# Kernel tuning notes

Measured on AMD Instinct MI355X. Metric: run time of the kernel, lower is better.

## Reference

```python
import jax, jax.numpy as jnp
import numpy as np

K = 32
BN_EPS = 1e-5


def _edgeconv(x, W, b):
    # x: [N, f] one point cloud; dynamic kNN in feature space (self included,
    # matching torch_geometric knn), edge feature [x_i, x_j - x_i], linear MLP,
    # max aggregation over the k neighbors.
    sq = jnp.sum(x * x, axis=1)                      # [N]
    dist = sq[:, None] + sq[None, :] - 2.0 * (x @ x.T)  # [N, N] squared dists
    _, idx = jax.lax.top_k(-dist, K)                 # [N, K] nearest (incl. self)
    xj = x[idx]                                      # [N, K, f]
    xi = jnp.broadcast_to(x[:, None, :], xj.shape)   # [N, K, f]
    e = jnp.concatenate([xi, xj - xi], axis=-1)      # [N, K, 2f]
    m = jnp.einsum('nkf,fo->nko', e, W) + b          # [N, K, o]
    return jnp.max(m, axis=1)                        # [N, o]


def _relu_bn(y, gamma, beta):
    # Sequential(ReLU(), BatchNorm1d(o)) in training mode over flattened nodes.
    a = jax.nn.relu(y)                               # [B, N, o]
    B, N, o = a.shape
    flat = a.reshape(B * N, o)
    mean = jnp.mean(flat, axis=0)
    var = jnp.var(flat, axis=0)
    norm = (flat - mean) * jax.lax.rsqrt(var + BN_EPS)
    return (norm * gamma + beta).reshape(B, N, o)


def setup_inputs() -> dict:
    key = jax.random.key(0)
    ks = jax.random.split(key, 4)
    B, N, fin = 8, 4096, 3
    x = jax.random.normal(ks[0], (B, N, fin), dtype=jnp.float32)
    target = jax.random.normal(ks[1], (B, N, fin), dtype=jnp.float32)
    # MLP(2*i, o) weights for layer dims (3->64), (64->64), (64->3)
    W1 = jax.random.normal(ks[2], (6, 64), dtype=jnp.float32) * (1.0 / np.sqrt(6))
    b1 = jnp.zeros((64,), jnp.float32)
    g1 = jnp.ones((64,), jnp.float32)
    be1 = jnp.zeros((64,), jnp.float32)
    W2 = jax.random.normal(ks[3], (128, 64), dtype=jnp.float32) * (1.0 / np.sqrt(128))
    b2 = jnp.zeros((64,), jnp.float32)
    g2 = jnp.ones((64,), jnp.float32)
    be2 = jnp.zeros((64,), jnp.float32)
    W3 = jax.random.normal(jax.random.fold_in(key, 7), (128, 3), dtype=jnp.float32) * (1.0 / np.sqrt(128))
    b3 = jnp.zeros((3,), jnp.float32)
    return {"x": x, "target": target, "W1": W1, "b1": b1, "g1": g1, "be1": be1,
            "W2": W2, "b2": b2, "g2": g2, "be2": be2, "W3": W3, "b3": b3}


def reference(x, target, W1, b1, g1, be1, W2, b2, g2, be2, W3, b3):
    ec = jax.vmap(_edgeconv, in_axes=(0, None, None))
    h = ec(x, W1, b1)                 # [B, N, 64]
    h = _relu_bn(h, g1, be1)
    h = ec(h, W2, b2)                 # [B, N, 64]
    h = _relu_bn(h, g2, be2)
    h = ec(h, W3, b3)                 # [B, N, 3], last activation = Identity
    loss = jnp.mean((h - target) ** 2)
    return (h, loss)
```

## Files before the change

### kernel.cpp

```cpp
#include <hip/hip_runtime.h>
#include <cstdint>
#include <cstddef>

static constexpr int NPTS  = 4096;
static constexpr int NB    = 8;
static constexpr int NROWS = NB * NPTS;
static constexpr int KNN   = 32;
static constexpr int CAP   = 384;
static constexpr int QCAP  = 96;

typedef __attribute__((ext_vector_type(8))) short  bf16x8;
typedef __attribute__((ext_vector_type(4))) float  f32x4;

__device__ __forceinline__ unsigned long long shfl_xor_u64(unsigned long long v, int m) {
  int lo = __shfl_xor((int)(unsigned)(v & 0xFFFFFFFFULL), m, 64);
  int hi = __shfl_xor((int)(unsigned)(v >> 32), m, 64);
  return ((unsigned long long)(unsigned)hi << 32) | (unsigned)lo;
}
__device__ __forceinline__ unsigned long long shfl_u64(unsigned long long v, int src) {
  int lo = __shfl((int)(unsigned)(v & 0xFFFFFFFFULL), src, 64);
  int hi = __shfl((int)(unsigned)(v >> 32), src, 64);
  return ((unsigned long long)(unsigned)hi << 32) | (unsigned)lo;
}

__device__ __forceinline__ unsigned f2o(float f) {
  unsigned u = __float_as_uint(f);
  return (u & 0x80000000u) ? ~u : (u | 0x80000000u);
}
__device__ __forceinline__ float o2f(unsigned o) {
  unsigned u = (o & 0x80000000u) ? (o ^ 0x80000000u) : ~o;
  return __uint_as_float(u);
}

__global__ __launch_bounds__(256) void sqnorm_kernel(const float* __restrict__ x,
                                                     float* __restrict__ sq, int F) {
  int t = blockIdx.x * 256 + threadIdx.x;
  if (t >= NROWS) return;
  const float* p = x + (size_t)t * F;
  float s = 0.f;
  for (int f = 0; f < F; ++f) s = fmaf(p[f], p[f], s);
  sq[t] = s;
}

__global__ __launch_bounds__(256) void split_kernel(const float* __restrict__ x,
                                                    unsigned short* __restrict__ hi,
                                                    unsigned short* __restrict__ lo,
                                                    int total) {
  int t = blockIdx.x * 256 + threadIdx.x;
  if (t >= total) return;
  float v = x[t];
  unsigned u = __float_as_uint(v);
  unsigned h = (u + 0x7FFFu + ((u >> 16) & 1u)) >> 16;
  float hf = __uint_as_float(h << 16);
  float r = v - hf;
  unsigned ur = __float_as_uint(r);
  unsigned l = (ur + 0x7FFFu + ((ur >> 16) & 1u)) >> 16;

  const int n = t >> 6;
  const int f = t & 63;
  const int b   = n >> 12;
  const int g   = (n >> 4) & 255;
  const int l16 = n & 15;
  const int p    = f >> 5;
  const int quad = (f >> 3) & 3;
  const int w    = f & 7;
  const size_t dst = ((((size_t)b * 256 + g) * 2 + p) << 9)
                   + (size_t)(quad * 16 + l16) * 8 + w;
  hi[dst] = (unsigned short)h;
  lo[dst] = (unsigned short)l;
}

__global__ __launch_bounds__(256) void batchmax_kernel(const float* __restrict__ sq,
                                                       float* __restrict__ sqmax) {
  int b = blockIdx.x, t = threadIdx.x;
  float m = 0.f;
  for (int i = t; i < NPTS; i += 256) m = fmaxf(m, sq[b * NPTS + i]);
  for (int off = 32; off >= 1; off >>= 1) m = fmaxf(m, __shfl_xor(m, off, 64));
  __shared__ float ls[4];
  if ((t & 63) == 0) ls[t >> 6] = m;
  __syncthreads();
  if (t == 0) sqmax[b] = fmaxf(fmaxf(ls[0], ls[1]), fmaxf(ls[2], ls[3]));
}

__global__ __launch_bounds__(256, 4)
void knn_screen(const unsigned short* __restrict__ hi,
                const unsigned short* __restrict__ lo,
                const float* __restrict__ sq,
                const float* __restrict__ sqmax,
                int* __restrict__ gcnt,
                unsigned short* __restrict__ glist) {
  const int t = threadIdx.x, wave = t >> 6, lane = t & 63;
  const int l16 = lane & 15, quad = lane >> 4;
  const int bid = blockIdx.x;
  const int b    = bid & 7;
  const int qtr  = (bid >> 3) & 3;
  const int i0w  = ((bid >> 5) << 6) + (wave << 4);
  const int cbq  = qtr << 10;
  const size_t base = (size_t)b * NPTS;
  const unsigned short* hib = hi + base * 64;
  const unsigned short* lob = lo + base * 64;
  const float* sqb = sq + base;
  const float sqm = sqmax[b];
  const int laneoff = lane * 8;

  bf16x8 ahi[2], alo[2];
#pragma unroll
  for (int kb = 0; kb < 2; ++kb) {
    const size_t abase = ((size_t)((i0w >> 4) * 2 + kb) << 9);
    ahi[kb] = *(const bf16x8*)(hib + abase + laneoff);
    alo[kb] = *(const bf16x8*)(lob + abase + laneoff);
  }
  float sqi4[4];
#pragma unroll
  for (int reg = 0; reg < 4; ++reg) sqi4[reg] = sqb[i0w + quad * 4 + reg];

  float t1[4], t2[4], t3[4], t4[4], tinf4[4];
  int cnt4[4] = {0, 0, 0, 0};
#pragma unroll
  for (int reg = 0; reg < 4; ++reg) {
    t1[reg] = 3.4e38f; t2[reg] = 3.4e38f; t3[reg] = 3.4e38f; t4[reg] = 3.4e38f;
    tinf4[reg] = 0.f;
  }

#pragma unroll 2
  for (int sub = 0; sub < 64; ++sub) {
    const size_t bb = ((size_t)((qtr * 64 + sub) * 2) << 9);
    bf16x8 bh0 = *(const bf16x8*)(hib + bb + laneoff);
    bf16x8 bh1 = *(const bf16x8*)(hib + bb + 512 + laneoff);
    bf16x8 bl0 = *(const bf16x8*)(lob + bb + laneoff);
    bf16x8 bl1 = *(const bf16x8*)(lob + bb + 512 + laneoff);
    f32x4 acc = {0.f, 0.f, 0.f, 0.f};
    acc = __builtin_amdgcn_mfma_f32_16x16x32_bf16(ahi[0], bh0, acc, 0, 0, 0);
    acc = __builtin_amdgcn_mfma_f32_16x16x32_bf16(ahi[1], bh1, acc, 0, 0, 0);
    acc = __builtin_amdgcn_mfma_f32_16x16x32_bf16(ahi[0], bl0, acc, 0, 0, 0);
    acc = __builtin_amdgcn_mfma_f32_16x16x32_bf16(ahi[1], bl1, acc, 0, 0, 0);
    acc = __builtin_amdgcn_mfma_f32_16x16x32_bf16(alo[0], bh0, acc, 0, 0, 0);
    acc = __builtin_amdgcn_mfma_f32_16x16x32_bf16(alo[1], bh1, acc, 0, 0, 0);
    const float cs = sqb[cbq + sub * 16 + l16];
#pragma unroll
    for (int reg = 0; reg < 4; ++reg) {
      float d = fmaf(-2.f, acc[reg], sqi4[reg] + cs);
      float m1 = fminf(d,  t1[reg]); float M1 = fmaxf(d,  t1[reg]);
      float m2 = fminf(M1, t2[reg]); float M2 = fmaxf(M1, t2[reg]);
      float m3 = fminf(M2, t3[reg]); float M3 = fmaxf(M2, t3[reg]);
      t1[reg] = m1; t2[reg] = m2; t3[reg] = m3;
      t4[reg] = fminf(M3, t4[reg]);
    }
  }

#pragma unroll
  for (int reg = 0; reg < 4; ++reg) {
    unsigned c0s = f2o(t1[reg]);
    unsigned c1s = f2o(t2[reg]);
    unsigned c2s = f2o(t3[reg]);
    unsigned c3s = f2o(t4[reg]);
    unsigned prefix = 0;
    int need = 32;
    for (int bit = 31; bit >= 0; --bit) {
      unsigned hm = (bit == 31) ? 0u : ~((1u << (bit + 1)) - 1u);
      bool a0 = (((c0s ^ prefix) & hm) == 0u) && (((c0s >> bit) & 1u) == 0u);
      bool a1 = (((c1s ^ prefix) & hm) == 0u) && (((c1s >> bit) & 1u) == 0u);
      bool a2 = (((c2s ^ prefix) & hm) == 0u) && (((c2s >> bit) & 1u) == 0u);
      bool a3 = (((c3s ^ prefix) & hm) == 0u) && (((c3s >> bit) & 1u) == 0u);
      unsigned long long b0 = __ballot(a0);
      unsigned long long b1 = __ballot(a1);
      unsigned long long b2 = __ballot(a2);
      unsigned long long b3 = __ballot(a3);
      int cnt0 = __popc((unsigned)((b0 >> (quad * 16)) & 0xFFFFULL))
               + __popc((unsigned)((b1 >> (quad * 16)) & 0xFFFFULL))
               + __popc((unsigned)((b2 >> (quad * 16)) & 0xFFFFULL))
               + __popc((unsigned)((b3 >> (quad * 16)) & 0xFFFFULL));
      if (cnt0 < need) { need -= cnt0; prefix |= 1u << bit; }
    }
    float T = o2f(prefix);
    float eps = 6e-5f * (sqi4[reg] + sqm) + 1e-5f;
    tinf4[reg] = T + 2.f * eps;
  }

#pragma unroll 2
  for (int sub = 0; sub < 64; ++sub) {
    const size_t bb = ((size_t)((qtr * 64 + sub) * 2) << 9);
    bf16x8 bh0 = *(const bf16x8*)(hib + bb + laneoff);
    bf16x8 bh1 = *(const bf16x8*)(hib + bb + 512 + laneoff);
    bf16x8 bl0 = *(const bf16x8*)(lob + bb + laneoff);
    bf16x8 bl1 = *(const bf16x8*)(lob + bb + 512 + laneoff);
    f32x4 acc = {0.f, 0.f, 0.f, 0.f};
    acc = __builtin_amdgcn_mfma_f32_16x16x32_bf16(ahi[0], bh0, acc, 0, 0, 0);
    acc = __builtin_amdgcn_mfma_f32_16x16x32_bf16(ahi[1], bh1, acc, 0, 0, 0);
    acc = __builtin_amdgcn_mfma_f32_16x16x32_bf16(ahi[0], bl0, acc, 0, 0, 0);
    acc = __builtin_amdgcn_mfma_f32_16x16x32_bf16(ahi[1], bl1, acc, 0, 0, 0);
    acc = __builtin_amdgcn_mfma_f32_16x16x32_bf16(alo[0], bh0, acc, 0, 0, 0);
    acc = __builtin_amdgcn_mfma_f32_16x16x32_bf16(alo[1], bh1, acc, 0, 0, 0);
    const int jg0 = cbq + sub * 16 + l16;
    const float cs = sqb[jg0];
#pragma unroll
    for (int reg = 0; reg < 4; ++reg) {
      float d = fmaf(-2.f, acc[reg], sqi4[reg] + cs);
      bool keep = d <= tinf4[reg];
      unsigned long long mask = __ballot(keep);
      unsigned qm = (unsigned)((mask >> (quad * 16)) & 0xFFFFULL);
      if (qm) {
        int rank = __popc(qm & ((1u << l16) - 1u));
        if (keep) {
          int pos = cnt4[reg] + rank;
          if (pos < QCAP)
            glist[(size_t)(base + i0w + quad * 4 + reg) * CAP + qtr * QCAP + pos] =
                (unsigned short)jg0;
        }
        cnt4[reg] += __popc(qm);
      }
    }
  }

  if (l16 == 0) {
#pragma unroll
    for (int reg = 0; reg < 4; ++reg)
      gcnt[(base + i0w + quad * 4 + reg) * 4 + qtr] = cnt4[reg];
  }
}

__global__ __launch_bounds__(256, 2)
void knn_rerank(const float* __restrict__ x, const float* __restrict__ sq,
                const int* __restrict__ gcnt,
                const unsigned short* __restrict__ glist,
                unsigned short* __restrict__ idx_out) {
  const int t = threadIdx.x, wave = t >> 6, lane = t & 63;
  const int row = blockIdx.x * 4 + wave;
  const int b = row >> 12;
  const int i = row & (NPTS - 1);
  const float* xb  = x + (size_t)b * NPTS * 64;
  const float* sqb = sq + ((size_t)b << 12);

  const int n0 = gcnt[row * 4 + 0];
  const int n1 = gcnt[row * 4 + 1];
  const int n2 = gcnt[row * 4 + 2];
  const int n3 = gcnt[row * 4 + 3];
  if (n0 > QCAP || n1 > QCAP || n2 > QCAP || n3 > QCAP) return;

  const float sqi = sqb[i];
  float4 q[16];
#pragma unroll
  for (int c4 = 0; c4 < 16; ++c4)
    q[c4] = *(const float4*)(xb + (size_t)i * 64 + c4 * 4);

  const int n01  = n0 + n1;
  const int n012 = n01 + n2;
  const int n    = n012 + n3;
  unsigned long long vk[6];
#pragma unroll
  for (int s = 0; s < 6; ++s) {
    int li = s * 64 + lane;
    unsigned long long v = 0xFFFFFFFFFFFULL;
    if (li < n) {
      int sl = (li < n0)   ? li
             : (li < n01)  ? QCAP     + (li - n0)
             : (li < n012) ? 2 * QCAP + (li - n01)
                           : 3 * QCAP + (li - n012);
      int j = glist[(size_t)row * CAP + sl];
      const float4* xj = (const float4*)(xb + (size_t)j * 64);
      float dot = 0.f;
#pragma unroll
      for (int c4 = 0; c4 < 16; ++c4) {
        float4 c = xj[c4];
        dot = fmaf(q[c4].x, c.x, dot);
        dot = fmaf(q[c4].y, c.y, dot);
        dot = fmaf(q[c4].z, c.z, dot);
        dot = fmaf(q[c4].w, c.w, dot);
      }
      float d = fmaf(-2.f, dot, sqi + sqb[j]);
      unsigned u  = __float_as_uint(d);
      unsigned ck = (u & 0x80000000u) ? ~u : (u | 0x80000000u);
      v = ((unsigned long long)ck << 12) | (unsigned)j;
    }
    vk[s] = v;
  }
  unsigned long long prefix = 0;
  int need = 32;
  for (int bit = 43; bit >= 0; --bit) {
    unsigned long long hm = (bit == 43) ? 0ULL
        : (~((1ULL << (bit + 1)) - 1ULL) & 0xFFFFFFFFFFFULL);
    int cnt0 = 0;
#pragma unroll
    for (int s = 0; s < 6; ++s) {
      bool a = ((vk[s] ^ prefix) & hm) == 0ULL;
      bool z = ((vk[s] >> bit) & 1ULL) == 0ULL;
      cnt0 += (int)__popcll(__ballot(a && z));
    }
    if (cnt0 < need) { need -= cnt0; prefix |= 1ULL << bit; }
  }
  int prev = 0;
#pragma unroll
  for (int s = 0; s < 6; ++s) {
    bool sel = vk[s] <= prefix;
    unsigned long long m = __ballot(sel);
    int rank = (int)__popcll(m & ((1ULL << lane) - 1ULL));
    if (sel)
      idx_out[(size_t)row * KNN + prev + rank] =
          (unsigned short)(vk[s] & 0xFFFULL);
    prev += (int)__popcll(m);
  }
}

__global__ __launch_bounds__(256)
void knn_rerank_fb(const float* __restrict__ x, const float* __restrict__ sq,
                   const int* __restrict__ gcnt,
                   unsigned short* __restrict__ idx_out) {
  __shared__ unsigned long long fsurv[4][128];
  const int t = threadIdx.x, wave = t >> 6, lane = t & 63;
  const int row = blockIdx.x * 4 + wave;
  const int b = row >> 12;
  const int i = row & (NPTS - 1);

  const int n0 = gcnt[row * 4 + 0];
  const int n1 = gcnt[row * 4 + 1];
  const int n2 = gcnt[row * 4 + 2];
  const int n3 = gcnt[row * 4 + 3];
  if (n0 <= QCAP && n1 <= QCAP && n2 <= QCAP && n3 <= QCAP) return;

  const float* xb  = x + (size_t)b * NPTS * 64;
  const float* sqb = sq + ((size_t)b << 12);
  const float sqi = sqb[i];

  float4 q[16];
#pragma unroll
  for (int c4 = 0; c4 < 16; ++c4)
    q[c4] = *(const float4*)(xb + (size_t)i * 64 + c4 * 4);

  unsigned mnf = 0xFFFFFFFFu;
  for (int c0 = 0; c0 < NPTS; c0 += 64) {
    const int j = c0 + lane;
    const float4* xj = (const float4*)(xb + (size_t)j * 64);
    float dot = 0.f;
#pragma unroll
    for (int c4 = 0; c4 < 16; ++c4) {
      float4 c = xj[c4];
      dot = fmaf(q[c4].x, c.x, dot);
      dot = fmaf(q[c4].y, c.y, dot);
      dot = fmaf(q[c4].z, c.z, dot);
      dot = fmaf(q[c4].w, c.w, dot);
    }
    float d = fmaf(-2.f, dot, sqi + sqb[j]);
    unsigned u  = __float_as_uint(d);
    unsigned ck = (u & 0x80000000u) ? ~u : (u | 0x80000000u);
    mnf = ck < mnf ? ck : mnf;
  }
  unsigned tau32;
  {
    const unsigned v = mnf;
    unsigned prefix32 = 0;
    int need = 32;
    int act = 1;
    for (int bit = 31; bit >= 0; --bit) {
      const unsigned bv = (v >> bit) & 1u;
      unsigned long long m0 = __ballot(act && (bv == 0u));
      int c0n = (int)__popcll(m0);
      if (c0n >= need) {
        act = act && (bv == 0u);
      } else {
        need -= c0n;
        act = act && (bv == 1u);
        prefix32 |= (1u << bit);
      }
    }
    tau32 = prefix32;
  }
  int cnt = 0;
  for (int c0 = 0; c0 < NPTS; c0 += 64) {
    const int j = c0 + lane;
    const float4* xj = (const float4*)(xb + (size_t)j * 64);
    float dot = 0.f;
#pragma unroll
    for (int c4 = 0; c4 < 16; ++c4) {
      float4 c = xj[c4];
      dot = fmaf(q[c4].x, c.x, dot);
      dot = fmaf(q[c4].y, c.y, dot);
      dot = fmaf(q[c4].z, c.z, dot);
      dot = fmaf(q[c4].w, c.w, dot);
    }
    float d = fmaf(-2.f, dot, sqi + sqb[j]);
    unsigned u  = __float_as_uint(d);
    unsigned ck = (u & 0x80000000u) ? ~u : (u | 0x80000000u);
    bool keep = ck <= tau32;
    unsigned long long mask = __ballot(keep);
    if (mask != 0ULL) {
      int rank = (int)__popcll(mask & ((1ULL << lane) - 1ULL));
      if (keep) {
        int pos = cnt + rank;
        if (pos < 128)
          fsurv[wave][pos] = ((unsigned long long)ck << 12) | (unsigned)j;
      }
      cnt += (int)__popcll(mask);
    }
  }
  if (cnt <= 128) {
    unsigned long long vk0 = (lane      < cnt) ? fsurv[wave][lane]      : 0xFFFFFFFFFFFULL;
    unsigned long long vk1 = (lane + 64 < cnt) ? fsurv[wave][lane + 64] : 0xFFFFFFFFFFFULL;
    unsigned long long prefix = 0;
    int need = 32;
    for (int bit = 43; bit >= 0; --bit) {
      unsigned long long hm = (bit == 43) ? 0ULL
          : (~((1ULL << (bit + 1)) - 1ULL) & 0xFFFFFFFFFFFULL);
      bool a0 = (((vk0 ^ prefix) & hm) == 0ULL) && (((vk0 >> bit) & 1ULL) == 0ULL);
      bool a1 = (((vk1 ^ prefix) & hm) == 0ULL) && (((vk1 >> bit) & 1ULL) == 0ULL);
      int cnt0 = (int)__popcll(__ballot(a0)) + (int)__popcll(__ballot(a1));
      if (cnt0 < need) { need -= cnt0; prefix |= 1ULL << bit; }
    }
    bool sel0 = vk0 <= prefix;
    unsigned long long m0 = __ballot(sel0);
    int rank0 = (int)__popcll(m0 & ((1ULL << lane) - 1ULL));
    if (sel0)
      idx_out[(size_t)row * KNN + rank0] = (unsigned short)(vk0 & 0xFFFULL);
    int prev = (int)__popcll(m0);
    bool sel1 = vk1 <= prefix;
    unsigned long long m1 = __ballot(sel1);
    int rank1 = (int)__popcll(m1 & ((1ULL << lane) - 1ULL));
    if (sel1)
      idx_out[(size_t)row * KNN + prev + rank1] = (unsigned short)(vk1 & 0xFFFULL);
  } else {
    unsigned long long ent = (0xFFFFFFFFFFFULL << 5) | (unsigned long long)(lane & 31);
    unsigned long long M   = (0xFFFFFFFFFFFULL << 5) | 31ULL;
    for (int c0 = 0; c0 < NPTS; c0 += 64) {
      const int j = c0 + lane;
      const float4* xj = (const float4*)(xb + (size_t)j * 64);
      float dot = 0.f;
#pragma unroll
      for (int c4 = 0; c4 < 16; ++c4) {
        float4 c = xj[c4];
        dot = fmaf(q[c4].x, c.x, dot);
        dot = fmaf(q[c4].y, c.y, dot);
        dot = fmaf(q[c4].z, c.z, dot);
        dot = fmaf(q[c4].w, c.w, dot);
      }
      float d = fmaf(-2.f, dot, sqi + sqb[j]);
      unsigned u  = __float_as_uint(d);
      unsigned ck = (u & 0x80000000u) ? ~u : (u | 0x80000000u);
      unsigned long long cq = ((unsigned long long)ck << 12) | (unsigned)j;
      unsigned long long mask = __ballot(cq < (M >> 5));
      while (mask) {
        const int src = __builtin_ctzll(mask);
        mask &= mask - 1;
        const unsigned long long bq = shfl_u64(cq, src);
        if (bq < (M >> 5)) {
          const unsigned slot = (unsigned)(M & 31ULL);
          if ((unsigned)(lane & 31) == slot) ent = (bq << 5) | slot;
          unsigned long long v = ent;
#pragma unroll
          for (int off = 16; off >= 1; off >>= 1) {
            unsigned long long w2 = shfl_xor_u64(v, off);
            v = (v > w2) ? v : w2;
          }
          M = v;
        }
      }
    }
    if (lane < 32)
      idx_out[(size_t)row * KNN + lane] =
          (unsigned short)((ent >> 5) & 0xFFFULL);
  }
}

template <int F>
__global__ __launch_bounds__(256, 4) void knn_tiled(const float* __restrict__ x,
                                                    const float* __restrict__ sq,
                                                    unsigned short* __restrict__ idx_out) {
  constexpr int FP = 4;
  constexpr int TC = 256;
  constexpr int RPB = 32;
  constexpr int RPW = 8;
  constexpr int SCAP = 128;

  __shared__ __attribute__((aligned(16))) float qv[RPB][FP];
  __shared__ float qsq[RPB];
  __shared__ __attribute__((aligned(16))) float ct[TC][FP];
  __shared__ float csq[TC];
  __shared__ unsigned long long surv[RPB][SCAP];

  const int t    = threadIdx.x;
  const int wave = t >> 6;
  const int lane = t & 63;
  const int rowbase = blockIdx.x << 5;
  const int b     = rowbase >> 12;
  const int ibase = rowbase & (NPTS - 1);
  const float* xb  = x + (size_t)b * NPTS * F;
  const float* sqb = sq + (b << 12);

  if (t < RPB) {
    qv[t][0] = xb[(size_t)(ibase + t) * 3 + 0];
    qv[t][1] = xb[(size_t)(ibase + t) * 3 + 1];
    qv[t][2] = xb[(size_t)(ibase + t) * 3 + 2];
    qv[t][3] = 0.f;
    qsq[t] = sqb[ibase + t];
  }
  __syncthreads();

  const int r0 = wave << 3;
  float4 q[RPW];
  float sqi[RPW];
#pragma unroll
  for (int rr = 0; rr < RPW; ++rr) {
    q[rr] = *reinterpret_cast<const float4*>(&qv[r0 + rr][0]);
    sqi[rr] = qsq[r0 + rr];
  }

  unsigned mn[RPW];
#pragma unroll
  for (int rr = 0; rr < RPW; ++rr) mn[rr] = 0xFFFFFFFFu;

  for (int tile = 0; tile < NPTS / TC; ++tile) {
    __syncthreads();
    {
      int jg = tile * TC + t;
      ct[t][0] = xb[(size_t)jg * 3 + 0];
      ct[t][1] = xb[(size_t)jg * 3 + 1];
      ct[t][2] = xb[(size_t)jg * 3 + 2];
      ct[t][3] = 0.f;
      csq[t] = sqb[jg];
    }
    __syncthreads();

    float4 c0 = *reinterpret_cast<const float4*>(&ct[lane][0]);
    float4 c1 = *reinterpret_cast<const float4*>(&ct[lane + 64][0]);
    float4 c2 = *reinterpret_cast<const float4*>(&ct[lane + 128][0]);
    float4 c3 = *reinterpret_cast<const float4*>(&ct[lane + 192][0]);
    float cs[4];
#pragma unroll
    for (int s = 0; s < 4; ++s) cs[s] = csq[lane + 64 * s];

#pragma unroll
    for (int rr = 0; rr < RPW; ++rr) {
      float4 qq = q[rr];
      float dd[4];
      dd[0] = fmaf(qq.z, c0.z, fmaf(qq.y, c0.y, qq.x * c0.x));
      dd[1] = fmaf(qq.z, c1.z, fmaf(qq.y, c1.y, qq.x * c1.x));
      dd[2] = fmaf(qq.z, c2.z, fmaf(qq.y, c2.y, qq.x * c2.x));
      dd[3] = fmaf(qq.z, c3.z, fmaf(qq.y, c3.y, qq.x * c3.x));
#pragma unroll
      for (int s = 0; s < 4; ++s) {
        float d = fmaf(-2.f, dd[s], sqi[rr] + cs[s]);
        unsigned u  = __float_as_uint(d);
        unsigned ck = (u & 0x80000000u) ? ~u : (u | 0x80000000u);
        mn[rr] = ck < mn[rr] ? ck : mn[rr];
      }
    }
  }

  unsigned tau[RPW];
#pragma unroll
  for (int rr = 0; rr < RPW; ++rr) {
    const unsigned v = mn[rr];
    unsigned prefix = 0;
    int need = 32;
    int act = 1;
    for (int bit = 31; bit >= 0; --bit) {
      const unsigned bv = (v >> bit) & 1u;
      unsigned long long m0 = __ballot(act && (bv == 0u));
      int c0n = (int)__popcll(m0);
      if (c0n >= need) {
        act = act && (bv == 0u);
      } else {
        need -= c0n;
        act = act && (bv == 1u);
        prefix |= (1u << bit);
      }
    }
    tau[rr] = prefix;
  }

  int cnt[RPW];
#pragma unroll
  for (int rr = 0; rr < RPW; ++rr) cnt[rr] = 0;

  for (int tile = 0; tile < NPTS / TC; ++tile) {
    __syncthreads();
    {
      int jg = tile * TC + t;
      ct[t][0] = xb[(size_t)jg * 3 + 0];
      ct[t][1] = xb[(size_t)jg * 3 + 1];
      ct[t][2] = xb[(size_t)jg * 3 + 2];
      ct[t][3] = 0.f;
      csq[t] = sqb[jg];
    }
    __syncthreads();

    float4 c0 = *reinterpret_cast<const float4*>(&ct[lane][0]);
    float4 c1 = *reinterpret_cast<const float4*>(&ct[lane + 64][0]);
    float4 c2 = *reinterpret_cast<const float4*>(&ct[lane + 128][0]);
    float4 c3 = *reinterpret_cast<const float4*>(&ct[lane + 192][0]);
    float cs[4];
#pragma unroll
    for (int s = 0; s < 4; ++s) cs[s] = csq[lane + 64 * s];

#pragma unroll
    for (int rr = 0; rr < RPW; ++rr) {
      float4 qq = q[rr];
      float dd[4];
      dd[0] = fmaf(qq.z, c0.z, fmaf(qq.y, c0.y, qq.x * c0.x));
      dd[1] = fmaf(qq.z, c1.z, fmaf(qq.y, c1.y, qq.x * c1.x));
      dd[2] = fmaf(qq.z, c2.z, fmaf(qq.y, c2.y, qq.x * c2.x));
      dd[3] = fmaf(qq.z, c3.z, fmaf(qq.y, c3.y, qq.x * c3.x));
#pragma unroll
      for (int s = 0; s < 4; ++s) {
        float d = fmaf(-2.f, dd[s], sqi[rr] + cs[s]);
        unsigned u  = __float_as_uint(d);
        unsigned ck = (u & 0x80000000u) ? ~u : (u | 0x80000000u);
        bool keep = ck <= tau[rr];
        unsigned long long mask = __ballot(keep);
        if (mask != 0ULL) {
          int rank = (int)__popcll(mask & ((1ULL << lane) - 1ULL));
          if (keep) {
            int pos = cnt[rr] + rank;
            if (pos < SCAP)
              surv[r0 + rr][pos] =
                  ((unsigned long long)ck << 12) |
                  (unsigned)(tile * TC + s * 64 + lane);
          }
          cnt[rr] += (int)__popcll(mask);
        }
      }
    }
  }

#pragma unroll
  for (int rr = 0; rr < RPW; ++rr) {
    const int row = rowbase + r0 + rr;
    const int n = cnt[rr];
    if (n <= SCAP) {
      unsigned long long vk0 = (lane      < n) ? surv[r0 + rr][lane]      : 0xFFFFFFFFFFFULL;
      unsigned long long vk1 = (lane + 64 < n) ? surv[r0 + rr][lane + 64] : 0xFFFFFFFFFFFULL;
      unsigned long long prefix = 0;
      int need = 32;
      for (int bit = 43; bit >= 0; --bit) {
        unsigned long long hm = (bit == 43) ? 0ULL
            : (~((1ULL << (bit + 1)) - 1ULL) & 0xFFFFFFFFFFFULL);
        bool a0 = (((vk0 ^ prefix) & hm) == 0ULL) && (((vk0 >> bit) & 1ULL) == 0ULL);
        bool a1 = (((vk1 ^ prefix) & hm) == 0ULL) && (((vk1 >> bit) & 1ULL) == 0ULL);
        int cnt0 = (int)__popcll(__ballot(a0)) + (int)__popcll(__ballot(a1));
        if (cnt0 < need) { need -= cnt0; prefix |= 1ULL << bit; }
      }
      bool sel0 = vk0 <= prefix;
      unsigned long long m0 = __ballot(sel0);
      int rank0 = (int)__popcll(m0 & ((1ULL << lane) - 1ULL));
      if (sel0)
        idx_out[(row << 5) + rank0] = (unsigned short)(vk0 & 0xFFFULL);
      int prev = (int)__popcll(m0);
      bool sel1 = vk1 <= prefix;
      unsigned long long m1 = __ballot(sel1);
      int rank1 = (int)__popcll(m1 & ((1ULL << lane) - 1ULL));
      if (sel1)
        idx_out[(row << 5) + prev + rank1] = (unsigned short)(vk1 & 0xFFFULL);
    } else {
      unsigned long long ent = (0xFFFFFFFFFFFULL << 5) | (unsigned long long)(lane & 31);
      unsigned long long M   = (0xFFFFFFFFFFFULL << 5) | 31ULL;
      const float4 qq = q[rr];
      const float si = sqi[rr];
      for (int c0i = 0; c0i < NPTS; c0i += 64) {
        const int j = c0i + lane;
        const float dd_ = fmaf(qq.z, xb[(size_t)j * 3 + 2],
                           fmaf(qq.y, xb[(size_t)j * 3 + 1],
                                qq.x * xb[(size_t)j * 3 + 0]));
        float d = fmaf(-2.f, dd_, si + sqb[j]);
        unsigned u  = __float_as_uint(d);
        unsigned ck = (u & 0x80000000u) ? ~u : (u | 0x80000000u);
        unsigned long long cq = ((unsigned long long)ck << 12) | (unsigned)j;
        unsigned long long mask = __ballot(cq < (M >> 5));
        while (mask) {
          const int src = __builtin_ctzll(mask);
          mask &= mask - 1;
          const unsigned long long bq = shfl_u64(cq, src);
          if (bq < (M >> 5)) {
            const unsigned slot = (unsigned)(M & 31ULL);
            if ((unsigned)(lane & 31) == slot) ent = (bq << 5) | slot;
            unsigned long long v = ent;
#pragma unroll
            for (int off = 16; off >= 1; off >>= 1) {
              unsigned long long w2 = shfl_xor_u64(v, off);
              v = (v > w2) ? v : w2;
            }
            M = v;
          }
        }
      }
      if (lane < 32)
        idx_out[(row << 5) + lane] = (unsigned short)((ent >> 5) & 0xFFFULL);
    }
  }
}

__global__ __launch_bounds__(256) void mlp_pc_kernel(const float* __restrict__ xin,
                                                     const float* __restrict__ W,
                                                     const float* __restrict__ bias,
                                                     float* __restrict__ P,
                                                     float* C,
                                                     int F, int O, int total) {
  int t = blockIdx.x * 256 + threadIdx.x;
  if (t >= total) return;
  int n = t / O, o = t % O;
  const float* xr = xin + (size_t)n * F;
  const float* Wt = W + o;
  const float* Wb = W + (size_t)F * O + o;
  float p = 0.f, c = 0.f;
  for (int f = 0; f < F; ++f) {
    float a  = xr[f];
    float wt = Wt[(size_t)f * O];
    float wb = Wb[(size_t)f * O];
    p = fmaf(a, wb, p);
    c = fmaf(a, wt - wb, c);
  }
  P[t] = p;
  C[t] = c + bias[o];
}

__global__ __launch_bounds__(256) void aggregate_kernel(const unsigned short* __restrict__ idx,
                                                        const float* __restrict__ P,
                                                        float* h, int O, int total) {
  int t = blockIdx.x * 256 + threadIdx.x;
  if (t >= total) return;
  int n = t / O, o = t % O;
  const unsigned short* ix = idx + (size_t)n * KNN;
  const int rowbase = (n >> 12) << 12;
  float m = -3.402823466e+38f;
  for (int k = 0; k < KNN; ++k) {
    int jg = rowbase + ix[k];
    float v = P[(size_t)jg * O + o];
    m = fmaxf(m, v);
  }
  h[t] = h[t] + m;
}

__global__ __launch_bounds__(256) void bn_stats_kernel(const float* __restrict__ h,
                                                       float* __restrict__ stats) {
  const int c = blockIdx.x;
  const int t = threadIdx.x;
  double s = 0.0, s2 = 0.0;
  for (int n = t; n < NROWS; n += 256) {
    float v = h[(size_t)n * 64 + c];
    v = v > 0.f ? v : 0.f;
    s += v;
    s2 += (double)v * v;
  }
  __shared__ double ls[256], ls2[256];
  ls[t] = s; ls2[t] = s2;
  __syncthreads();
  for (int st = 128; st; st >>= 1) {
    if (t < st) { ls[t] += ls[t + st]; ls2[t] += ls2[t + st]; }
    __syncthreads();
  }
  if (t == 0) {
    double mean = ls[0] / (double)NROWS;
    double var  = ls2[0] / (double)NROWS - mean * mean;
    stats[c]      = (float)mean;
    stats[64 + c] = (float)(1.0 / sqrt(var + 1e-5));
  }
}

__global__ __launch_bounds__(256) void bn_apply_kernel(const float* h,
                                                       const float* __restrict__ stats,
                                                       const float* __restrict__ g,
                                                       const float* __restrict__ be,
                                                       float* out, int total) {
  int t = blockIdx.x * 256 + threadIdx.x;
  if (t >= total) return;
  int ch = t & 63;
  float v = fmaxf(h[t], 0.f);
  out[t] = (v - stats[ch]) * stats[64 + ch] * g[ch] + be[ch];
}

__global__ __launch_bounds__(256) void final_kernel(const float* __restrict__ h3,
                                                    const float* __restrict__ target,
                                                    float* __restrict__ out,
                                                    double* __restrict__ partial) {
  double s = 0.0;
  for (int t = blockIdx.x * 256 + threadIdx.x; t < NROWS * 3; t += 256 * 256) {
    float v = h3[t];
    out[t] = v;
    float d = v - target[t];
    s += (double)d * d;
  }
  __shared__ double ls[256];
  int t = threadIdx.x;
  ls[t] = s;
  __syncthreads();
  for (int st = 128; st; st >>= 1) {
    if (t < st) ls[t] += ls[t + st];
    __syncthreads();
  }
  if (t == 0) partial[blockIdx.x] = ls[0];
}

__global__ __launch_bounds__(256) void loss_kernel(const double* __restrict__ partial,
                                                   float* __restrict__ out) {
  int t = threadIdx.x;
  __shared__ double ls[256];
  ls[t] = partial[t];
  __syncthreads();
  for (int st = 128; st; st >>= 1) {
    if (t < st) ls[t] += ls[t + st];
    __syncthreads();
  }
  if (t == 0) out[NROWS * 3] = (float)(ls[0] / (double)(NROWS * 3));
}

extern "C" void kernel_launch(void* const* d_in, const int* in_sizes, int n_in,
                              void* d_out, int out_size, void* d_ws, size_t ws_size,
                              hipStream_t stream) {
  const float* x   = (const float*)d_in[0];
  const float* tgt = (const float*)d_in[1];
  const float* W1  = (const float*)d_in[2];
  const float* b1  = (const float*)d_in[3];
  const float* g1  = (const float*)d_in[4];
  const float* be1 = (const float*)d_in[5];
  const float* W2  = (const float*)d_in[6];
  const float* b2  = (const float*)d_in[7];
  const float* g2  = (const float*)d_in[8];
  const float* be2 = (const float*)d_in[9];
  const float* W3  = (const float*)d_in[10];
  const float* b3  = (const float*)d_in[11];
  float* out = (float*)d_out;

  char* ws = (char*)d_ws;
  size_t off = 0;
  float* sq    = (float*)(ws + off); off += (size_t)NROWS * 4;
  unsigned short* idxb = (unsigned short*)(ws + off); off += (size_t)NROWS * KNN * 2;
  float* P     = (float*)(ws + off); off += (size_t)NROWS * 64 * 4;
  float* CA    = (float*)(ws + off); off += (size_t)NROWS * 64 * 4;
  float* CB    = (float*)(ws + off); off += (size_t)NROWS * 64 * 4;
  int*   gcnt  = (int*)(ws + off);   off += (size_t)NROWS * 16;
  unsigned short* glist = (unsigned short*)(ws + off); off += (size_t)NROWS * CAP * 2;
  float* stats = (float*)(ws + off); off += 256 * 4;
  float* sqmax = (float*)(ws + off); off += 64;
  double* part = (double*)(ws + off); off += 256 * 8;

  unsigned short* hib = (unsigned short*)P;
  unsigned short* lob = hib + (size_t)NROWS * 64;

  const int T64 = NROWS * 64;
  const int T3  = NROWS * 3;

  sqnorm_kernel<<<NROWS / 256, 256, 0, stream>>>(x, sq, 3);
  knn_tiled<3><<<NROWS / 32, 256, 0, stream>>>(x, sq, idxb);
  mlp_pc_kernel<<<T64 / 256, 256, 0, stream>>>(x, W1, b1, P, CA, 3, 64, T64);
  aggregate_kernel<<<T64 / 256, 256, 0, stream>>>(idxb, P, CA, 64, T64);
  bn_stats_kernel<<<64, 256, 0, stream>>>(CA, stats);
  bn_apply_kernel<<<T64 / 256, 256, 0, stream>>>(CA, stats, g1, be1, CA, T64);

  sqnorm_kernel<<<NROWS / 256, 256, 0, stream>>>(CA, sq, 64);
  split_kernel<<<T64 / 256, 256, 0, stream>>>(CA, hib, lob, T64);
  batchmax_kernel<<<NB, 256, 0, stream>>>(sq, sqmax);
  knn_screen<<<2048, 256, 0, stream>>>(hib, lob, sq, sqmax, gcnt, glist);
  knn_rerank<<<NROWS / 4, 256, 0, stream>>>(CA, sq, gcnt, glist, idxb);
  knn_rerank_fb<<<NROWS / 4, 256, 0, stream>>>(CA, sq, gcnt, idxb);
  mlp_pc_kernel<<<T64 / 256, 256, 0, stream>>>(CA, W2, b2, P, CB, 64, 64, T64);
  aggregate_kernel<<<T64 / 256, 256, 0, stream>>>(idxb, P, CB, 64, T64);
  bn_stats_kernel<<<64, 256, 0, stream>>>(CB, stats);
  bn_apply_kernel<<<T64 / 256, 256, 0, stream>>>(CB, stats, g2, be2, CB, T64);

  sqnorm_kernel<<<NROWS / 256, 256, 0, stream>>>(CB, sq, 64);
  split_kernel<<<T64 / 256, 256, 0, stream>>>(CB, hib, lob, T64);
  batchmax_kernel<<<NB, 256, 0, stream>>>(sq, sqmax);
  knn_screen<<<2048, 256, 0, stream>>>(hib, lob, sq, sqmax, gcnt, glist);
  knn_rerank<<<NROWS / 4, 256, 0, stream>>>(CB, sq, gcnt, glist, idxb);
  knn_rerank_fb<<<NROWS / 4, 256, 0, stream>>>(CB, sq, gcnt, idxb);
  mlp_pc_kernel<<<T3 / 256, 256, 0, stream>>>(CB, W3, b3, P, CA, 64, 3, T3);
  aggregate_kernel<<<T3 / 256, 256, 0, stream>>>(idxb, P, CA, 3, T3);

  final_kernel<<<256, 256, 0, stream>>>(CA, tgt, out, part);
  loss_kernel<<<1, 256, 0, stream>>>(part, out);
}
```

Baseline: 1.478 ms.

## Split kNN candidate screening into halves instead of quarters

The screening kernel now splits the candidate columns into two halves of 2048 points instead of four quarters of 1024. Each query row then keeps a top-4-per-lane threshold over more candidates. That gives a tighter cut, so fewer candidates survive into a smaller 256-slot list, and the rerank kernel scans fewer slots. The trade-offs are half as many blocks, each with twice the loop length, which lowers parallelism. Rows that overflow the 128-slot per-half capacity fall back to the slow full-scan path, so the fallback may be taken more often.

```diff
diff --git a/kernel.cpp b/kernel.cpp
--- a/kernel.cpp
+++ b/kernel.cpp
@@ -6,8 +6,8 @@
 static constexpr int NB    = 8;
 static constexpr int NROWS = NB * NPTS;
 static constexpr int KNN   = 32;
-static constexpr int CAP   = 384;
-static constexpr int QCAP  = 96;
+static constexpr int CAP   = 256;
+static constexpr int HCAP  = 128;
 
 typedef __attribute__((ext_vector_type(8))) short  bf16x8;
 typedef __attribute__((ext_vector_type(4))) float  f32x4;
@@ -93,9 +93,9 @@
   const int l16 = lane & 15, quad = lane >> 4;
   const int bid = blockIdx.x;
   const int b    = bid & 7;
-  const int qtr  = (bid >> 3) & 3;
-  const int i0w  = ((bid >> 5) << 6) + (wave << 4);
-  const int cbq  = qtr << 10;
+  const int half = (bid >> 3) & 1;
+  const int i0w  = ((bid >> 4) << 6) + (wave << 4);
+  const int cbh  = half << 11;
   const size_t base = (size_t)b * NPTS;
   const unsigned short* hib = hi + base * 64;
   const unsigned short* lob = lo + base * 64;
@@ -123,8 +123,8 @@
   }
 
 #pragma unroll 2
-  for (int sub = 0; sub < 64; ++sub) {
-    const size_t bb = ((size_t)((qtr * 64 + sub) * 2) << 9);
+  for (int sub = 0; sub < 128; ++sub) {
+    const size_t bb = ((size_t)((half * 128 + sub) * 2) << 9);
     bf16x8 bh0 = *(const bf16x8*)(hib + bb + laneoff);
     bf16x8 bh1 = *(const bf16x8*)(hib + bb + 512 + laneoff);
     bf16x8 bl0 = *(const bf16x8*)(lob + bb + laneoff);
@@ -136,7 +136,7 @@
     acc = __builtin_amdgcn_mfma_f32_16x16x32_bf16(ahi[1], bl1, acc, 0, 0, 0);
     acc = __builtin_amdgcn_mfma_f32_16x16x32_bf16(alo[0], bh0, acc, 0, 0, 0);
     acc = __builtin_amdgcn_mfma_f32_16x16x32_bf16(alo[1], bh1, acc, 0, 0, 0);
-    const float cs = sqb[cbq + sub * 16 + l16];
+    const float cs = sqb[cbh + sub * 16 + l16];
 #pragma unroll
     for (int reg = 0; reg < 4; ++reg) {
       float d = fmaf(-2.f, acc[reg], sqi4[reg] + cs);
@@ -178,8 +178,8 @@
   }
 
 #pragma unroll 2
-  for (int sub = 0; sub < 64; ++sub) {
-    const size_t bb = ((size_t)((qtr * 64 + sub) * 2) << 9);
+  for (int sub = 0; sub < 128; ++sub) {
+    const size_t bb = ((size_t)((half * 128 + sub) * 2) << 9);
     bf16x8 bh0 = *(const bf16x8*)(hib + bb + laneoff);
     bf16x8 bh1 = *(const bf16x8*)(hib + bb + 512 + laneoff);
     bf16x8 bl0 = *(const bf16x8*)(lob + bb + laneoff);
@@ -191,7 +191,7 @@
     acc = __builtin_amdgcn_mfma_f32_16x16x32_bf16(ahi[1], bl1, acc, 0, 0, 0);
     acc = __builtin_amdgcn_mfma_f32_16x16x32_bf16(alo[0], bh0, acc, 0, 0, 0);
     acc = __builtin_amdgcn_mfma_f32_16x16x32_bf16(alo[1], bh1, acc, 0, 0, 0);
-    const int jg0 = cbq + sub * 16 + l16;
+    const int jg0 = cbh + sub * 16 + l16;
     const float cs = sqb[jg0];
 #pragma unroll
     for (int reg = 0; reg < 4; ++reg) {
@@ -203,8 +203,8 @@
         int rank = __popc(qm & ((1u << l16) - 1u));
         if (keep) {
           int pos = cnt4[reg] + rank;
-          if (pos < QCAP)
-            glist[(size_t)(base + i0w + quad * 4 + reg) * CAP + qtr * QCAP + pos] =
+          if (pos < HCAP)
+            glist[(size_t)(base + i0w + quad * 4 + reg) * CAP + half * HCAP + pos] =
                 (unsigned short)jg0;
         }
         cnt4[reg] += __popc(qm);
@@ -215,7 +215,7 @@
   if (l16 == 0) {
 #pragma unroll
     for (int reg = 0; reg < 4; ++reg)
-      gcnt[(base + i0w + quad * 4 + reg) * 4 + qtr] = cnt4[reg];
+      gcnt[(base + i0w + quad * 4 + reg) * 2 + half] = cnt4[reg];
   }
 }
 
@@ -231,11 +231,9 @@
   const float* xb  = x + (size_t)b * NPTS * 64;
   const float* sqb = sq + ((size_t)b << 12);
 
-  const int n0 = gcnt[row * 4 + 0];
-  const int n1 = gcnt[row * 4 + 1];
-  const int n2 = gcnt[row * 4 + 2];
-  const int n3 = gcnt[row * 4 + 3];
-  if (n0 > QCAP || n1 > QCAP || n2 > QCAP || n3 > QCAP) return;
+  const int n0 = gcnt[row * 2];
+  const int n1 = gcnt[row * 2 + 1];
+  if (n0 > HCAP || n1 > HCAP) return;
 
   const float sqi = sqb[i];
   float4 q[16];
@@ -243,19 +241,14 @@
   for (int c4 = 0; c4 < 16; ++c4)
     q[c4] = *(const float4*)(xb + (size_t)i * 64 + c4 * 4);
 
-  const int n01  = n0 + n1;
-  const int n012 = n01 + n2;
-  const int n    = n012 + n3;
-  unsigned long long vk[6];
-#pragma unroll
-  for (int s = 0; s < 6; ++s) {
+  const int n = n0 + n1;
+  unsigned long long vk[4];
+#pragma unroll
+  for (int s = 0; s < 4; ++s) {
     int li = s * 64 + lane;
     unsigned long long v = 0xFFFFFFFFFFFULL;
     if (li < n) {
-      int sl = (li < n0)   ? li
-             : (li < n01)  ? QCAP     + (li - n0)
-             : (li < n012) ? 2 * QCAP + (li - n01)
-                           : 3 * QCAP + (li - n012);
+      int sl = (li < n0) ? li : (HCAP + (li - n0));
       int j = glist[(size_t)row * CAP + sl];
       const float4* xj = (const float4*)(xb + (size_t)j * 64);
       float dot = 0.f;
@@ -281,7 +274,7 @@
         : (~((1ULL << (bit + 1)) - 1ULL) & 0xFFFFFFFFFFFULL);
     int cnt0 = 0;
 #pragma unroll
-    for (int s = 0; s < 6; ++s) {
+    for (int s = 0; s < 4; ++s) {
       bool a = ((vk[s] ^ prefix) & hm) == 0ULL;
       bool z = ((vk[s] >> bit) & 1ULL) == 0ULL;
       cnt0 += (int)__popcll(__ballot(a && z));
@@ -290,7 +283,7 @@
   }
   int prev = 0;
 #pragma unroll
-  for (int s = 0; s < 6; ++s) {
+  for (int s = 0; s < 4; ++s) {
     bool sel = vk[s] <= prefix;
     unsigned long long m = __ballot(sel);
     int rank = (int)__popcll(m & ((1ULL << lane) - 1ULL));
@@ -311,11 +304,9 @@
   const int b = row >> 12;
   const int i = row & (NPTS - 1);
 
-  const int n0 = gcnt[row * 4 + 0];
-  const int n1 = gcnt[row * 4 + 1];
-  const int n2 = gcnt[row * 4 + 2];
-  const int n3 = gcnt[row * 4 + 3];
-  if (n0 <= QCAP && n1 <= QCAP && n2 <= QCAP && n3 <= QCAP) return;
+  const int n0 = gcnt[row * 2];
+  const int n1 = gcnt[row * 2 + 1];
+  if (n0 <= HCAP && n1 <= HCAP) return;
 
   const float* xb  = x + (size_t)b * NPTS * 64;
   const float* sqb = sq + ((size_t)b << 12);
@@ -824,7 +815,7 @@
   float* P     = (float*)(ws + off); off += (size_t)NROWS * 64 * 4;
   float* CA    = (float*)(ws + off); off += (size_t)NROWS * 64 * 4;
   float* CB    = (float*)(ws + off); off += (size_t)NROWS * 64 * 4;
-  int*   gcnt  = (int*)(ws + off);   off += (size_t)NROWS * 16;
+  int*   gcnt  = (int*)(ws + off);   off += (size_t)NROWS * 8;
   unsigned short* glist = (unsigned short*)(ws + off); off += (size_t)NROWS * CAP * 2;
   float* stats = (float*)(ws + off); off += 256 * 4;
   float* sqmax = (float*)(ws + off); off += 64;
@@ -846,7 +837,7 @@
   sqnorm_kernel<<<NROWS / 256, 256, 0, stream>>>(CA, sq, 64);
   split_kernel<<<T64 / 256, 256, 0, stream>>>(CA, hib, lob, T64);
   batchmax_kernel<<<NB, 256, 0, stream>>>(sq, sqmax);
-  knn_screen<<<2048, 256, 0, stream>>>(hib, lob, sq, sqmax, gcnt, glist);
+  knn_screen<<<1024, 256, 0, stream>>>(hib, lob, sq, sqmax, gcnt, glist);
   knn_rerank<<<NROWS / 4, 256, 0, stream>>>(CA, sq, gcnt, glist, idxb);
   knn_rerank_fb<<<NROWS / 4, 256, 0, stream>>>(CA, sq, gcnt, idxb);
   mlp_pc_kernel<<<T64 / 256, 256, 0, stream>>>(CA, W2, b2, P, CB, 64, 64, T64);
@@ -857,7 +848,7 @@
   sqnorm_kernel<<<NROWS / 256, 256, 0, stream>>>(CB, sq, 64);
   split_kernel<<<T64 / 256, 256, 0, stream>>>(CB, hib, lob, T64);
   batchmax_kernel<<<NB, 256, 0, stream>>>(sq, sqmax);
-  knn_screen<<<2048, 256, 0, stream>>>(hib, lob, sq, sqmax, gcnt, glist);
+  knn_screen<<<1024, 256, 0, stream>>>(hib, lob, sq, sqmax, gcnt, glist);
   knn_rerank<<<NROWS / 4, 256, 0, stream>>>(CB, sq, gcnt, glist, idxb);
   knn_rerank_fb<<<NROWS / 4, 256, 0, stream>>>(CB, sq, gcnt, idxb);
   mlp_pc_kernel<<<T3 / 256, 256, 0, stream>>>(CB, W3, b3, P, CA, 64, 3, T3);
```

After: 1.254 ms (median of 2 runs). 15.1% less time.
